# Optimization experiments

Hardware: AMD Instinct MI355X
Metric: run time of the kernel (lower is better)

Reference implementation:

```python
import jax, jax.numpy as jnp
import numpy as np
import math

B, N, OBS, H, A = 4096, 64, 64, 64, 8


def setup_inputs() -> dict:
    key = jax.random.key(0)
    kit = iter(jax.random.split(key, 64))

    def W(o, i):
        return jax.random.normal(next(kit), (o, i), jnp.float32) / float(np.sqrt(i))

    def bvec(o):
        return jax.random.normal(next(kit), (o,), jnp.float32) * 0.01

    inp = {
        "x": jax.random.normal(next(kit), (B, N, OBS), jnp.float32),
        "rnd_nums": jax.random.uniform(next(kit), (B, N), dtype=jnp.float32),
        "idx": jax.random.randint(next(kit), (B, N), 0, N),
    }
    inp.update(embed_w=W(H, OBS), embed_b=bvec(H))
    for pre in ("ia", "c1", "c2"):  # init_attn, consensus_attn1, consensus_attn2 (1 head)
        inp.update({pre + "_wq": W(H, H), pre + "_bq": bvec(H),
                    pre + "_wk": W(H, H), pre + "_bk": bvec(H),
                    pre + "_wv": W(H, H), pre + "_bv": bvec(H),
                    pre + "_wo": W(H, H), pre + "_bo": bvec(H)})
    inp.update(msg_w=W(H, H), msg_b=bvec(H), st_w=W(H, H), st_b=bvec(H),
               mean_w=W(A, 2 * H), mean_b=bvec(A), ls_w=W(A, 2 * H), ls_b=bvec(A))
    return inp


def reference(x, rnd_nums, idx, embed_w, embed_b,
              ia_wq, ia_bq, ia_wk, ia_bk, ia_wv, ia_bv, ia_wo, ia_bo,
              msg_w, msg_b, st_w, st_b,
              c1_wq, c1_bq, c1_wk, c1_bk, c1_wv, c1_bv, c1_wo, c1_bo,
              c2_wq, c2_bq, c2_wk, c2_bk, c2_wv, c2_bv, c2_wo, c2_bo,
              mean_w, mean_b, ls_w, ls_b):
    h = embed_w.shape[0]
    scale = 1.0 / math.sqrt(h)
    lrelu = lambda z: jax.nn.leaky_relu(z, 0.2)

    # ---- initial state estimation (self-attention over agents) ----
    e = lrelu(x @ embed_w.T + embed_b)                       # [B,N,H]
    q = e @ ia_wq.T + ia_bq
    k = e @ ia_wk.T + ia_bk
    v = e @ ia_wv.T + ia_bv
    w = jax.nn.softmax(jnp.einsum('bih,bjh->bij', q, k) * scale, axis=-1)
    attn = jnp.tanh(jnp.einsum('bij,bjh->bih', w, v) @ ia_wo.T + ia_bo)
    messages = attn @ msg_w.T + msg_b                        # [B,N,H]
    temp = attn @ st_w.T + st_b                              # [B,N,H]

    # ---- consensus masks: mg[b,i,j] = (r_i > a_i) | (r_j > a_i) ----
    a = jnp.take_along_axis(rnd_nums, idx, axis=1)           # agent_rnd per agent slot [B,N]
    gi = rnd_nums[:, :, None] > a[:, :, None]
    gj = rnd_nums[:, None, :] > a[:, :, None]
    mg = (gi | gj).astype(x.dtype)                           # [B,N,N]
    ml = 1.0 - mg

    def cons(mask, wq, bq, wk, bk, wv, bv, wo, bo):
        # single-token query (agent temp state) attends over zero-masked messages;
        # masked tokens contribute k = bk, v = bv (bias survives the zeroing).
        qq = temp @ wq.T + bq                                # [B,N,H]
        km = messages @ wk.T                                 # [B,N,H] (no bias; folded below)
        vm = messages @ wv.T
        s = (mask * jnp.einsum('bih,bjh->bij', qq, km) + (qq @ bk)[:, :, None]) * scale
        wgt = jax.nn.softmax(s, axis=-1)                     # [B,N_agents,N_tokens]
        ctx = jnp.einsum('bij,bjh->bih', wgt * mask, vm) + bv
        return ctx @ wo.T + bo

    o1 = cons(mg, c1_wq, c1_bq, c1_wk, c1_bk, c1_wv, c1_bv, c1_wo, c1_bo)
    o2 = cons(ml, c2_wq, c2_bq, c2_wk, c2_bk, c2_wv, c2_bv, c2_wo, c2_bo)
    out = lrelu(jnp.concatenate([o1, o2], axis=-1))          # [B,N,2H]
    mean = out @ mean_w.T + mean_b                           # [B,N,A]
    logstd = jnp.clip(out @ ls_w.T + ls_b, -20.0, 2.0)
    return mean, jnp.exp(logstd)
```

## Files before the change

### kernel.cpp

```cpp
#include <hip/hip_runtime.h>

namespace {

typedef __bf16 bf16x8 __attribute__((ext_vector_type(8)));
typedef float f32x4 __attribute__((ext_vector_type(4)));
typedef unsigned int uint4v __attribute__((ext_vector_type(4)));

#define MFMA16(a,b,c) __builtin_amdgcn_mfma_f32_16x16x32_bf16((a),(b),(c),0,0,0)

constexpr float SCALE = 0.125f;

constexpr int WS_HW  = 57344;
constexpr int WS_NV  = 61440;
constexpr int WS_VEC = 63488;
constexpr int WS_SC  = 65536;

__device__ __forceinline__ int PI(int c){ return 4*(c&15) + (c>>4); }
__device__ __forceinline__ int PINV(int p){ return 16*(p&3) + (p>>2); }

__device__ __forceinline__ unsigned short f2b(float f){
  return __builtin_bit_cast(unsigned short, (__bf16)f);
}
__device__ __forceinline__ unsigned pack2(float a, float b){
  return (unsigned)f2b(a) | ((unsigned)f2b(b)<<16);
}
template<int ACT>
__device__ __forceinline__ float actf(float v){
  if constexpr (ACT==1) return v>0.f ? v : 0.2f*v;
  else if constexpr (ACT==2) return 1.f - 2.f/(__expf(2.f*v)+1.f);
  else return v;
}

__device__ __forceinline__ void bar_lgkm(){
  asm volatile("s_waitcnt lgkmcnt(0)\n\ts_barrier" ::: "memory");
}
__device__ __forceinline__ void bar_full(){
  asm volatile("s_waitcnt vmcnt(0) lgkmcnt(0)\n\ts_barrier" ::: "memory");
}

struct PrepP {
  const float *embed_w, *mean_w, *ls_w;
  const float *ia_wq, *ia_bq, *ia_wk, *ia_wv, *ia_wo, *ia_bv, *ia_bo;
  const float *c1_wq, *c1_bq, *c1_wk, *c1_bk, *c1_wv, *c1_bv, *c1_wo, *c1_bo;
  const float *c2_wq, *c2_bq, *c2_wk, *c2_bk, *c2_wv, *c2_bv, *c2_wo, *c2_bo;
  const float *msg_w, *msg_b, *st_w, *st_b;
  char* ws;
};

__device__ void mmAB_f32(const float* A, const float* B, float* O){
  const int t=threadIdx.x, r=t>>2, c0=(t&3)*16;
  float acc[16];
  #pragma unroll
  for(int j=0;j<16;j++) acc[j]=0.f;
  for(int h=0;h<64;h++){
    const float a=A[r*64+h];
    #pragma unroll
    for(int j=0;j<16;j++) acc[j]=fmaf(a,B[h*64+c0+j],acc[j]);
  }
  #pragma unroll
  for(int j=0;j<16;j++) O[r*64+c0+j]=acc[j];
}
__device__ void mmAB_bf(const float* A, const float* B, __bf16* D){
  const int t=threadIdx.x, r=t>>2, c0=(t&3)*16;
  float acc[16];
  #pragma unroll
  for(int j=0;j<16;j++) acc[j]=0.f;
  for(int h=0;h<64;h++){
    const float a=A[r*64+h];
    #pragma unroll
    for(int j=0;j<16;j++) acc[j]=fmaf(a,B[h*64+c0+j],acc[j]);
  }
  #pragma unroll
  for(int j=0;j<16;j++) D[r*64+PI(c0+j)]=(__bf16)acc[j];
}
__device__ void mmTA_bfx(const float* A, const float* B, __bf16* D){
  const int t=threadIdx.x, a=t>>2, b0=(t&3)*16;
  float acc[16];
  #pragma unroll
  for(int j=0;j<16;j++) acc[j]=0.f;
  for(int h=0;h<64;h++){
    const float av=A[h*64+a];
    #pragma unroll
    for(int j=0;j<16;j++) acc[j]=fmaf(av,B[h*64+b0+j],acc[j]);
  }
  #pragma unroll
  for(int j=0;j<16;j++) D[a*64 + (PI(b0+j) ^ ((a&7)<<3))]=(__bf16)acc[j];
}

__global__ void prep_kernel(PrepP q){
  __shared__ float PF[2][4096];
  __shared__ float hv[64], gv[64];
  const int job=blockIdx.x, t=threadIdx.x;
  char* ws=q.ws;
  float* VECF=(float*)(ws+WS_VEC);
  float* SCF =(float*)(ws+WS_SC);
  __bf16* NVD=(__bf16*)(ws+WS_NV);

  if(job==0){
    __bf16* emb=(__bf16*)(ws+0*8192);
    #pragma unroll
    for(int i=0;i<16;i++){
      const int idx=t*16+i, o=idx>>6, pp=idx&63;
      emb[idx]=(__bf16)q.embed_w[o*64 + PINV(pp ^ ((o&7)<<3))];
    }
    __bf16* hw=(__bf16*)(ws+WS_HW);
    #pragma unroll
    for(int i=0;i<8;i++){
      const int flat=t*8+i, o=flat>>7, qq=flat&127, half=qq>>6, pp=qq&63;
      const float v=(o<8)?q.mean_w[o*128+half*64+PINV(pp)]
                         :q.ls_w[(o-8)*128+half*64+PINV(pp)];
      hw[flat]=(__bf16)v;
    }
    #pragma unroll
    for(int i=0;i<3;i++){ const int id=t*3+i; if(id<768) NVD[256+id]=(__bf16)0.f; }
  } else if(job==1){
    mmTA_bfx(q.ia_wk, q.ia_wq, (__bf16*)(ws+1*8192));
    if(t<64){ float s=0; for(int h=0;h<64;h++) s+=q.ia_wk[h*64+t]*q.ia_bq[h]; VECF[t]=s; }
  } else if(job==2){
    mmAB_bf(q.ia_wo, q.ia_wv, (__bf16*)(ws+2*8192));
    if(t<64){ float s=q.ia_bo[t]; for(int h=0;h<64;h++) s+=q.ia_wo[t*64+h]*q.ia_bv[h];
              VECF[64+t]=s; }
  } else if(job==3 || job==5){
    const int cons=(job==3)?0:1;
    const float *wq=cons?q.c2_wq:q.c1_wq, *bq=cons?q.c2_bq:q.c1_bq;
    const float *wk=cons?q.c2_wk:q.c1_wk, *bk=cons?q.c2_bk:q.c1_bk;
    mmAB_f32(wq, q.st_w, PF[0]);
    if(t<64){ float s=bq[t]; for(int k=0;k<64;k++) s+=wq[t*64+k]*q.st_b[k]; hv[t]=s; }
    __syncthreads();
    mmAB_f32(wk, q.msg_w, PF[1]);
    if(t<64){ float s=0; for(int k=0;k<64;k++) s+=wk[t*64+k]*q.msg_b[k]; gv[t]=s; }
    __syncthreads();
    mmTA_bfx(PF[1], PF[0], (__bf16*)(ws+(cons?5:3)*8192));
    if(t<64){
      float s=0; for(int h=0;h<64;h++) s+=PF[1][h*64+t]*hv[h];
      VECF[128+cons*64+t]=s;
      float s0=0,s1=0;
      for(int h=0;h<64;h++){ s0+=PF[0][h*64+t]*gv[h]; s1+=PF[0][h*64+t]*bk[h]; }
      NVD[(2*cons  )*64+PI(t)]=(__bf16)s0;
      NVD[(2*cons+1)*64+PI(t)]=(__bf16)s1;
    }
    if(t==0){
      float c=0,hb=0;
      for(int i=0;i<64;i++){ c+=hv[i]*gv[i]; hb+=hv[i]*bk[i]; }
      SCF[2*cons]=c; SCF[2*cons+1]=hb;
    }
  } else {
    const int cons=(job==4)?0:1;
    const float *wo=cons?q.c2_wo:q.c1_wo, *wvv=cons?q.c2_wv:q.c1_wv;
    const float *bv=cons?q.c2_bv:q.c1_bv, *bo=cons?q.c2_bo:q.c1_bo;
    mmAB_f32(wo, wvv, PF[0]);
    if(t<64){ float s=bo[t]; for(int h=0;h<64;h++) s+=wo[t*64+h]*bv[h];
              VECF[320+cons*128+t]=s; }
    __syncthreads();
    mmAB_bf(PF[0], q.msg_w, (__bf16*)(ws+(cons?6:4)*8192));
    if(t<64){ float s=0; for(int k=0;k<64;k++) s+=PF[0][t*64+k]*q.msg_b[k];
              VECF[256+cons*128+t]=s; }
  }
}

struct Params {
  const float *x, *rnd; const int *idx;
  const float *embed_b, *mean_b, *ls_b;
  const char* ws; float* out; int std_off;
};

__device__ __forceinline__ bf16x8 fragld(const char* buf, int row, int kb){
  const int byte = row*128 + (kb ^ ((row&7)<<4));
  return __builtin_bit_cast(bf16x8, *reinterpret_cast<const uint4v*>(buf + byte));
}
__device__ __forceinline__ bf16x8 gld(const char* a){
  return __builtin_bit_cast(bf16x8, *reinterpret_cast<const uint4v*>(a));
}
__device__ __forceinline__ void stageT(const char* src, char* L, int t){
  __builtin_amdgcn_global_load_lds(
      (const __attribute__((address_space(1))) unsigned int*)(src + t*16),
      (__attribute__((address_space(3))) unsigned int*)(L + (t>>6)*1024), 16, 0, 0);
}
__device__ __forceinline__ void loadB_lds(const char* Bl, bf16x8* bf, int fr, int fg){
  #pragma unroll
  for(int n=0;n<4;n++){
    bf[2*n]   = fragld(Bl, n*16+fr, fg*16);
    bf[2*n+1] = fragld(Bl, n*16+fr, 64+fg*16);
  }
}

__device__ __forceinline__ void mm_AB(const char* A, const char* Bl, f32x4* acc,
                                      int fr,int fg,int wv4){
  const bf16x8 a0=fragld(A,16*wv4+fr,fg*16), a1=fragld(A,16*wv4+fr,64+fg*16);
  #pragma unroll
  for(int n=0;n<4;n++){
    acc[n]=MFMA16(a0, fragld(Bl,n*16+fr,fg*16),    acc[n]);
    acc[n]=MFMA16(a1, fragld(Bl,n*16+fr,64+fg*16), acc[n]);
  }
}
__device__ __forceinline__ void mm_rAB(bf16x8 a0, bf16x8 a1, const bf16x8* bf,
                                       f32x4* acc){
  #pragma unroll
  for(int n=0;n<4;n++){
    acc[n]=MFMA16(a0, bf[2*n],   acc[n]);
    acc[n]=MFMA16(a1, bf[2*n+1], acc[n]);
  }
}

template<int ACT>
__device__ __forceinline__ void store_cb(char* C, const f32x4* acc, const float* bz,
                                         int fr,int fg,int wv4){
  #pragma unroll
  for(int r=0;r<4;r++){
    const int R=16*wv4+4*fg+r;
    float v[4];
    #pragma unroll
    for(int n=0;n<4;n++) v[n]=actf<ACT>(acc[n][r]+bz[n]);
    uint2 pk; pk.x=pack2(v[0],v[1]); pk.y=pack2(v[2],v[3]);
    *reinterpret_cast<uint2*>(C + R*128 + ((8*fr)^((R&7)<<4))) = pk;
  }
}
__device__ __forceinline__ void store_rb(char* C, const f32x4* acc, const float* dR,
                                         int fr,int fg,int wv4){
  #pragma unroll
  for(int r=0;r<4;r++){
    const int R=16*wv4+4*fg+r;
    float v[4];
    #pragma unroll
    for(int n=0;n<4;n++) v[n]=acc[n][r]+dR[r];
    uint2 pk; pk.x=pack2(v[0],v[1]); pk.y=pack2(v[2],v[3]);
    *reinterpret_cast<uint2*>(C + R*128 + ((8*fr)^((R&7)<<4))) = pk;
  }
}

template<int MODE>
__device__ __forceinline__ void ssoft(const char* Aq, const bf16x8* bf, char* P,
                                      const float* rs, const float* as_,
                                      const float* zu, const float* zq,
                                      float cu, float cq,
                                      int fr,int fg,int wv4){
  f32x4 acc[4];
  #pragma unroll
  for(int n=0;n<4;n++) acc[n]=f32x4{0.f,0.f,0.f,0.f};
  const bf16x8 a0=fragld(Aq,16*wv4+fr,fg*16), a1=fragld(Aq,16*wv4+fr,64+fg*16);
  #pragma unroll
  for(int n=0;n<4;n++){
    acc[n]=MFMA16(a0, bf[2*n],   acc[n]);
    acc[n]=MFMA16(a1, bf[2*n+1], acc[n]);
  }
  unsigned mbits=0;
  if constexpr(MODE!=0){
    float rc[4], aR[4], ucR[4], qtR[4]; bool giR[4];
    #pragma unroll
    for(int n=0;n<4;n++) rc[n]=rs[n*16+fr];
    #pragma unroll
    for(int r=0;r<4;r++){
      const int R=16*wv4+4*fg+r;
      aR[r]=as_[R]; giR[r]=rs[R]>aR[r];
      ucR[r]=zu[R]+cu; qtR[r]=zq[R]+cq;
    }
    #pragma unroll
    for(int n=0;n<4;n++){
      #pragma unroll
      for(int r=0;r<4;r++){
        bool mv=giR[r]||(rc[n]>aR[r]);
        if constexpr(MODE==2) mv=!mv;
        const float mf=mv?1.f:0.f;
        if(mv) mbits|=1u<<(n*4+r);
        acc[n][r]=(mf*(acc[n][r]+ucR[r])+qtR[r])*SCALE;
      }
    }
  }
  float sm[4]={0,0,0,0};
  #pragma unroll
  for(int n=0;n<4;n++){
    #pragma unroll
    for(int r=0;r<4;r++){
      float e;
      if constexpr(MODE==0) e=__expf(acc[n][r]*SCALE);
      else e=__expf(acc[n][r]);
      acc[n][r]=e; sm[r]+=e;
    }
  }
  #pragma unroll
  for(int m=1;m<16;m<<=1){
    #pragma unroll
    for(int r=0;r<4;r++) sm[r]+=__shfl_xor(sm[r],m);
  }
  #pragma unroll
  for(int r=0;r<4;r++){
    const int R=16*wv4+4*fg+r;
    const float ri=1.f/sm[r];
    float v[4];
    #pragma unroll
    for(int n=0;n<4;n++){
      float e=acc[n][r]*ri;
      if constexpr(MODE!=0) e=(mbits&(1u<<(n*4+r)))?e:0.f;
      v[n]=e;
    }
    uint2 pk; pk.x=pack2(v[0],v[1]); pk.y=pack2(v[2],v[3]);
    *reinterpret_cast<uint2*>(P + R*128 + ((8*fr)^((R&7)<<4))) = pk;
  }
}

__global__ __launch_bounds__(512,4) void rap_kernel(Params p, int Bb){
  __shared__ __align__(16) char Bact[2][3][8192];
  __shared__ __align__(16) char WSst[2][8192];
  __shared__ float rnd_s[2][64], a_s[2][64], zbuf[2][4][64];
  const int t=threadIdx.x;
  const int fr=t&15, fg=(t>>4)&3, wv=t>>6, l=t&63;
  const int item=wv>>2, wv4=wv&3;
  const int b0=blockIdx.x*2;
  const int bi=(b0+item<Bb)?(b0+item):(Bb-1);
  const char* ws=p.ws;
  const float* VECF=(const float*)(ws+WS_VEC);
  const float* SCF =(const float*)(ws+WS_SC);
  char* A0=Bact[item][0]; char* A1=Bact[item][1]; char* A2=Bact[item][2];
  char* WO1=WSst[item];
  bf16x8 bfv[8];

  stageT(ws+0*8192, WSst[0], t);
  stageT(ws+1*8192, WSst[1], t);
  if(t<128){
    const int it2=t>>6, i2=t&63;
    const int bb=(b0+it2<Bb)?(b0+it2):(Bb-1);
    rnd_s[it2][i2]=p.rnd[bb*64+i2];
    a_s[it2][i2]  =p.rnd[bb*64+p.idx[bb*64+i2]];
  }
  {
    const float* Gx=p.x+(size_t)bi*4096;
    #pragma unroll
    for(int j=0;j<2;j++){
      const int lf=j*64+l, R=16*wv4+(lf>>3), k=lf&7;
      const float2 L0=*reinterpret_cast<const float2*>(Gx+R*64+2*k);
      const float2 L1=*reinterpret_cast<const float2*>(Gx+R*64+16+2*k);
      const float2 L2=*reinterpret_cast<const float2*>(Gx+R*64+32+2*k);
      const float2 L3=*reinterpret_cast<const float2*>(Gx+R*64+48+2*k);
      uint4 pk;
      pk.x=pack2(L0.x,L1.x); pk.y=pack2(L2.x,L3.x);
      pk.z=pack2(L0.y,L1.y); pk.w=pack2(L2.y,L3.y);
      *reinterpret_cast<uint4*>(A0 + R*128 + ((16*k)^((R&7)<<4)))=pk;
    }
  }
  bar_full();
  { f32x4 acc[4]={{0,0,0,0},{0,0,0,0},{0,0,0,0},{0,0,0,0}};
    mm_AB(A0, WSst[0], acc, fr,fg,wv4);
    float bz[4];
    #pragma unroll
    for(int n=0;n<4;n++) bz[n]=p.embed_b[n*16+fr];
    store_cb<1>(A1, acc, bz, fr,fg,wv4); }
  { f32x4 acc[4]={{0,0,0,0},{0,0,0,0},{0,0,0,0},{0,0,0,0}};
    mm_AB(A1, WSst[1], acc, fr,fg,wv4);
    float bz[4];
    #pragma unroll
    for(int n=0;n<4;n++) bz[n]=VECF[n*16+fr];
    store_cb<0>(A0, acc, bz, fr,fg,wv4); }
  bar_lgkm();
  stageT(ws+3*8192, WSst[0], t);
  stageT(ws+5*8192, WSst[1], t);
  const bf16x8 aVo0=gld(ws+2*8192+(16*wv4+fr)*128+fg*16);
  const bf16x8 aVo1=gld(ws+2*8192+(16*wv4+fr)*128+64+fg*16);
  loadB_lds(A1, bfv, fr, fg);
  ssoft<0>(A0, bfv, A0, nullptr,nullptr,nullptr,nullptr,0.f,0.f, fr,fg,wv4);
  { f32x4 acc[4]={{0,0,0,0},{0,0,0,0},{0,0,0,0},{0,0,0,0}};
    mm_rAB(aVo0, aVo1, bfv, acc);
    const float bz[4]={0,0,0,0};
    store_cb<0>(A2, acc, bz, fr,fg,wv4); }
  bar_full();
  const bf16x8 nv0=gld(ws+WS_NV+fr*128+fg*16);
  const bf16x8 nv1=gld(ws+WS_NV+fr*128+64+fg*16);
  { f32x4 acc[4]={{0,0,0,0},{0,0,0,0},{0,0,0,0},{0,0,0,0}};
    mm_AB(A0, A2, acc, fr,fg,wv4);
    float bz[4];
    #pragma unroll
    for(int n=0;n<4;n++) bz[n]=VECF[64+n*16+fr];
    store_cb<2>(A1, acc, bz, fr,fg,wv4); }
  { const bf16x8 a0=fragld(A1,16*wv4+fr,fg*16), a1=fragld(A1,16*wv4+fr,64+fg*16);
    f32x4 acc[4]={{0,0,0,0},{0,0,0,0},{0,0,0,0},{0,0,0,0}};
    #pragma unroll
    for(int n=0;n<4;n++){
      acc[n]=MFMA16(a0, fragld(WSst[0],n*16+fr,fg*16),    acc[n]);
      acc[n]=MFMA16(a1, fragld(WSst[0],n*16+fr,64+fg*16), acc[n]);
    }
    f32x4 za={0,0,0,0};
    za=MFMA16(a0, nv0, za);
    za=MFMA16(a1, nv1, za);
    if(fr<4){
      #pragma unroll
      for(int r=0;r<4;r++) zbuf[item][fr][16*wv4+4*fg+r]=za[r];
    }
    float bz[4];
    #pragma unroll
    for(int n=0;n<4;n++) bz[n]=VECF[128+n*16+fr];
    store_cb<0>(A0, acc, bz, fr,fg,wv4); }
  bar_lgkm();
  const bf16x8 aN10=gld(ws+4*8192+(16*wv4+fr)*128+fg*16);
  const bf16x8 aN11=gld(ws+4*8192+(16*wv4+fr)*128+64+fg*16);
  loadB_lds(A1, bfv, fr, fg);
  ssoft<1>(A0, bfv, A0, rnd_s[item], a_s[item], zbuf[item][0], zbuf[item][1],
           SCF[0], SCF[1], fr,fg,wv4);
  { f32x4 acc[4]={{0,0,0,0},{0,0,0,0},{0,0,0,0},{0,0,0,0}};
    mm_rAB(aN10, aN11, bfv, acc);
    float dR[4];
    #pragma unroll
    for(int r=0;r<4;r++) dR[r]=VECF[256+16*wv4+4*fg+r];
    store_rb(A2, acc, dR, fr,fg,wv4); }
  bar_lgkm();
  f32x4 o1acc[4]={{0,0,0,0},{0,0,0,0},{0,0,0,0},{0,0,0,0}};
  mm_AB(A0, A2, o1acc, fr,fg,wv4);
  { f32x4 acc[4]={{0,0,0,0},{0,0,0,0},{0,0,0,0},{0,0,0,0}};
    const bf16x8 a0=fragld(A1,16*wv4+fr,fg*16), a1=fragld(A1,16*wv4+fr,64+fg*16);
    #pragma unroll
    for(int n=0;n<4;n++){
      acc[n]=MFMA16(a0, fragld(WSst[1],n*16+fr,fg*16),    acc[n]);
      acc[n]=MFMA16(a1, fragld(WSst[1],n*16+fr,64+fg*16), acc[n]);
    }
    float bz[4];
    #pragma unroll
    for(int n=0;n<4;n++) bz[n]=VECF[192+n*16+fr];
    store_cb<0>(A0, acc, bz, fr,fg,wv4); }
  bar_lgkm();
  { float bz[4];
    #pragma unroll
    for(int n=0;n<4;n++) bz[n]=VECF[320+n*16+fr];
    store_cb<1>(WO1, o1acc, bz, fr,fg,wv4); }
  const bf16x8 aN20=gld(ws+6*8192+(16*wv4+fr)*128+fg*16);
  const bf16x8 aN21=gld(ws+6*8192+(16*wv4+fr)*128+64+fg*16);
  loadB_lds(A1, bfv, fr, fg);
  ssoft<2>(A0, bfv, A0, rnd_s[item], a_s[item], zbuf[item][2], zbuf[item][3],
           SCF[2], SCF[3], fr,fg,wv4);
  { f32x4 acc[4]={{0,0,0,0},{0,0,0,0},{0,0,0,0},{0,0,0,0}};
    mm_rAB(aN20, aN21, bfv, acc);
    float dR[4];
    #pragma unroll
    for(int r=0;r<4;r++) dR[r]=VECF[384+16*wv4+4*fg+r];
    store_rb(A2, acc, dR, fr,fg,wv4); }
  bar_lgkm();
  bf16x8 hw[4];
  #pragma unroll
  for(int kt=0;kt<4;kt++) hw[kt]=gld(ws+WS_HW + fr*256 + kt*64 + fg*16);
  { f32x4 acc[4]={{0,0,0,0},{0,0,0,0},{0,0,0,0},{0,0,0,0}};
    mm_AB(A0, A2, acc, fr,fg,wv4);
    float bz[4];
    #pragma unroll
    for(int n=0;n<4;n++) bz[n]=VECF[448+n*16+fr];
    store_cb<1>(A1, acc, bz, fr,fg,wv4); }
  { f32x4 acc={0,0,0,0};
    #pragma unroll
    for(int kt=0;kt<4;kt++){
      const bf16x8 af=fragld(kt<2?WO1:A1, 16*wv4+fr, (kt&1)*64+fg*16);
      acc=MFMA16(af, hw[kt], acc);
    }
    if(b0+item<Bb){
      const float bz=(fr<8)?p.mean_b[fr]:p.ls_b[fr-8];
      #pragma unroll
      for(int r=0;r<4;r++){
        const int R=16*wv4+4*fg+r;
        const int g=((b0+item)*64+R)*8;
        float v=acc[r]+bz;
        if(fr<8) p.out[g+fr]=v;
        else{ v=fminf(fmaxf(v,-20.f),2.f); p.out[p.std_off+g+(fr-8)]=__expf(v); }
      }
    }
  }
}

}

extern "C" void kernel_launch(void* const* d_in, const int* in_sizes, int n_in,
                              void* d_out, int out_size, void* d_ws, size_t ws_size,
                              hipStream_t stream){
  (void)n_in; (void)out_size; (void)ws_size;
  PrepP q;
  q.embed_w=(const float*)d_in[3];
  q.ia_wq=(const float*)d_in[5];  q.ia_bq=(const float*)d_in[6];
  q.ia_wk=(const float*)d_in[7];
  q.ia_wv=(const float*)d_in[9];  q.ia_bv=(const float*)d_in[10];
  q.ia_wo=(const float*)d_in[11]; q.ia_bo=(const float*)d_in[12];
  q.c1_wq=(const float*)d_in[13]; q.c1_bq=(const float*)d_in[14];
  q.c1_wk=(const float*)d_in[15]; q.c1_bk=(const float*)d_in[16];
  q.c1_wv=(const float*)d_in[17]; q.c1_bv=(const float*)d_in[18];
  q.c1_wo=(const float*)d_in[19]; q.c1_bo=(const float*)d_in[20];
  q.c2_wq=(const float*)d_in[21]; q.c2_bq=(const float*)d_in[22];
  q.c2_wk=(const float*)d_in[23]; q.c2_bk=(const float*)d_in[24];
  q.c2_wv=(const float*)d_in[25]; q.c2_bv=(const float*)d_in[26];
  q.c2_wo=(const float*)d_in[27]; q.c2_bo=(const float*)d_in[28];
  q.msg_w=(const float*)d_in[29]; q.msg_b=(const float*)d_in[30];
  q.st_w =(const float*)d_in[31]; q.st_b =(const float*)d_in[32];
  q.mean_w=(const float*)d_in[33]; q.ls_w=(const float*)d_in[35];
  q.ws=(char*)d_ws;
  prep_kernel<<<dim3(7), dim3(256), 0, stream>>>(q);

  Params p;
  p.x  =(const float*)d_in[0];
  p.rnd=(const float*)d_in[1];
  p.idx=(const int*)  d_in[2];
  p.embed_b=(const float*)d_in[4];
  p.mean_b =(const float*)d_in[34];
  p.ls_b   =(const float*)d_in[36];
  p.ws=(const char*)d_ws;
  p.out=(float*)d_out;
  const int Bb=in_sizes[0]/4096;
  p.std_off=Bb*64*8;
  const int nb=(Bb+1)/2;
  rap_kernel<<<dim3(nb), dim3(512), 0, stream>>>(p, Bb);
}
```

Measured before the change: 115.8 us.

## Drop shared weight staging buffers, load consensus weights from global into registers

Removes the 16KB WSst shared buffer by staging the embed weights into the unused third activation slot, and loads consensus Q·K weight fragments straight from global into registers instead of LDS. The final head projection is split so the o1 part accumulates early, which frees the separate o1 buffer. Launch bounds go from 4 to 6 blocks per CU to use the reduced LDS footprint. The prep kernel's mmTA_bfx is replaced with an explicit per-thread loop that writes a permuted layout. This trades more global/L2 loads and register pressure for higher occupancy.

```diff
diff --git a/kernel.cpp b/kernel.cpp
--- a/kernel.cpp
+++ b/kernel.cpp
@@ -130,7 +130,19 @@
     mmAB_f32(wk, q.msg_w, PF[1]);
     if(t<64){ float s=0; for(int k=0;k<64;k++) s+=wk[t*64+k]*q.msg_b[k]; gv[t]=s; }
     __syncthreads();
-    mmTA_bfx(PF[1], PF[0], (__bf16*)(ws+(cons?5:3)*8192));
+    { const int a=t>>2, b0=(t&3)*16;
+      float acc[16];
+      #pragma unroll
+      for(int j=0;j<16;j++) acc[j]=0.f;
+      for(int h=0;h<64;h++){
+        const float av=PF[1][h*64+a];
+        #pragma unroll
+        for(int j=0;j<16;j++) acc[j]=fmaf(av,PF[0][h*64+b0+j],acc[j]);
+      }
+      __bf16* D=(__bf16*)(ws+(cons?5:3)*8192);
+      #pragma unroll
+      for(int j=0;j<16;j++) D[a*64+PI(b0+j)]=(__bf16)acc[j];
+    }
     if(t<64){
       float s=0; for(int h=0;h<64;h++) s+=PF[1][h*64+t]*hv[h];
       VECF[128+cons*64+t]=s;
@@ -183,6 +195,13 @@
     bf[2*n+1] = fragld(Bl, n*16+fr, 64+fg*16);
   }
 }
+__device__ __forceinline__ void loadB_gl(const char* W, bf16x8* bf, int fr, int fg){
+  #pragma unroll
+  for(int n=0;n<4;n++){
+    bf[2*n]   = gld(W + (n*16+fr)*128 + fg*16);
+    bf[2*n+1] = gld(W + (n*16+fr)*128 + 64 + fg*16);
+  }
+}
 
 __device__ __forceinline__ void mm_AB(const char* A, const char* Bl, f32x4* acc,
                                       int fr,int fg,int wv4){
@@ -191,6 +210,15 @@
   for(int n=0;n<4;n++){
     acc[n]=MFMA16(a0, fragld(Bl,n*16+fr,fg*16),    acc[n]);
     acc[n]=MFMA16(a1, fragld(Bl,n*16+fr,64+fg*16), acc[n]);
+  }
+}
+__device__ __forceinline__ void mm_ABr(const char* A, const bf16x8* bf, f32x4* acc,
+                                       int fr,int fg,int wv4){
+  const bf16x8 a0=fragld(A,16*wv4+fr,fg*16), a1=fragld(A,16*wv4+fr,64+fg*16);
+  #pragma unroll
+  for(int n=0;n<4;n++){
+    acc[n]=MFMA16(a0, bf[2*n],   acc[n]);
+    acc[n]=MFMA16(a1, bf[2*n+1], acc[n]);
   }
 }
 __device__ __forceinline__ void mm_rAB(bf16x8 a0, bf16x8 a1, const bf16x8* bf,
@@ -298,9 +326,8 @@
   }
 }
 
-__global__ __launch_bounds__(512,4) void rap_kernel(Params p, int Bb){
+__global__ __launch_bounds__(512,6) void rap_kernel(Params p, int Bb){
   __shared__ __align__(16) char Bact[2][3][8192];
-  __shared__ __align__(16) char WSst[2][8192];
   __shared__ float rnd_s[2][64], a_s[2][64], zbuf[2][4][64];
   const int t=threadIdx.x;
   const int fr=t&15, fg=(t>>4)&3, wv=t>>6, l=t&63;
@@ -311,11 +338,10 @@
   const float* VECF=(const float*)(ws+WS_VEC);
   const float* SCF =(const float*)(ws+WS_SC);
   char* A0=Bact[item][0]; char* A1=Bact[item][1]; char* A2=Bact[item][2];
-  char* WO1=WSst[item];
   bf16x8 bfv[8];
 
-  stageT(ws+0*8192, WSst[0], t);
-  stageT(ws+1*8192, WSst[1], t);
+  stageT(ws+0*8192, Bact[0][2], t);
+  stageT(ws+1*8192, Bact[1][2], t);
   if(t<128){
     const int it2=t>>6, i2=t&63;
     const int bb=(b0+it2<Bb)?(b0+it2):(Bb-1);
@@ -339,20 +365,18 @@
   }
   bar_full();
   { f32x4 acc[4]={{0,0,0,0},{0,0,0,0},{0,0,0,0},{0,0,0,0}};
-    mm_AB(A0, WSst[0], acc, fr,fg,wv4);
+    mm_AB(A0, Bact[0][2], acc, fr,fg,wv4);
     float bz[4];
     #pragma unroll
     for(int n=0;n<4;n++) bz[n]=p.embed_b[n*16+fr];
     store_cb<1>(A1, acc, bz, fr,fg,wv4); }
   { f32x4 acc[4]={{0,0,0,0},{0,0,0,0},{0,0,0,0},{0,0,0,0}};
-    mm_AB(A1, WSst[1], acc, fr,fg,wv4);
+    mm_AB(A1, Bact[1][2], acc, fr,fg,wv4);
     float bz[4];
     #pragma unroll
     for(int n=0;n<4;n++) bz[n]=VECF[n*16+fr];
     store_cb<0>(A0, acc, bz, fr,fg,wv4); }
   bar_lgkm();
-  stageT(ws+3*8192, WSst[0], t);
-  stageT(ws+5*8192, WSst[1], t);
   const bf16x8 aVo0=gld(ws+2*8192+(16*wv4+fr)*128+fg*16);
   const bf16x8 aVo1=gld(ws+2*8192+(16*wv4+fr)*128+64+fg*16);
   loadB_lds(A1, bfv, fr, fg);
@@ -361,9 +385,10 @@
     mm_rAB(aVo0, aVo1, bfv, acc);
     const float bz[4]={0,0,0,0};
     store_cb<0>(A2, acc, bz, fr,fg,wv4); }
-  bar_full();
+  bar_lgkm();
   const bf16x8 nv0=gld(ws+WS_NV+fr*128+fg*16);
   const bf16x8 nv1=gld(ws+WS_NV+fr*128+64+fg*16);
+  loadB_gl(ws+3*8192, bfv, fr, fg);
   { f32x4 acc[4]={{0,0,0,0},{0,0,0,0},{0,0,0,0},{0,0,0,0}};
     mm_AB(A0, A2, acc, fr,fg,wv4);
     float bz[4];
@@ -374,8 +399,8 @@
     f32x4 acc[4]={{0,0,0,0},{0,0,0,0},{0,0,0,0},{0,0,0,0}};
     #pragma unroll
     for(int n=0;n<4;n++){
-      acc[n]=MFMA16(a0, fragld(WSst[0],n*16+fr,fg*16),    acc[n]);
-      acc[n]=MFMA16(a1, fragld(WSst[0],n*16+fr,64+fg*16), acc[n]);
+      acc[n]=MFMA16(a0, bfv[2*n],   acc[n]);
+      acc[n]=MFMA16(a1, bfv[2*n+1], acc[n]);
     }
     f32x4 za={0,0,0,0};
     za=MFMA16(a0, nv0, za);
@@ -401,24 +426,25 @@
     for(int r=0;r<4;r++) dR[r]=VECF[256+16*wv4+4*fg+r];
     store_rb(A2, acc, dR, fr,fg,wv4); }
   bar_lgkm();
-  f32x4 o1acc[4]={{0,0,0,0},{0,0,0,0},{0,0,0,0},{0,0,0,0}};
-  mm_AB(A0, A2, o1acc, fr,fg,wv4);
-  { f32x4 acc[4]={{0,0,0,0},{0,0,0,0},{0,0,0,0},{0,0,0,0}};
-    const bf16x8 a0=fragld(A1,16*wv4+fr,fg*16), a1=fragld(A1,16*wv4+fr,64+fg*16);
-    #pragma unroll
-    for(int n=0;n<4;n++){
-      acc[n]=MFMA16(a0, fragld(WSst[1],n*16+fr,fg*16),    acc[n]);
-      acc[n]=MFMA16(a1, fragld(WSst[1],n*16+fr,64+fg*16), acc[n]);
-    }
+  loadB_gl(ws+5*8192, bfv, fr, fg);
+  const bf16x8 h0=gld(ws+WS_HW + fr*256 + 0*64 + fg*16);
+  const bf16x8 h1=gld(ws+WS_HW + fr*256 + 1*64 + fg*16);
+  f32x4 hacc={0,0,0,0};
+  { f32x4 o1acc[4]={{0,0,0,0},{0,0,0,0},{0,0,0,0},{0,0,0,0}};
+    mm_AB(A0, A2, o1acc, fr,fg,wv4);
+    float bz[4];
+    #pragma unroll
+    for(int n=0;n<4;n++) bz[n]=VECF[320+n*16+fr];
+    store_cb<1>(A0, o1acc, bz, fr,fg,wv4); }
+  hacc=MFMA16(fragld(A0,16*wv4+fr,fg*16),    h0, hacc);
+  hacc=MFMA16(fragld(A0,16*wv4+fr,64+fg*16), h1, hacc);
+  { f32x4 acc[4]={{0,0,0,0},{0,0,0,0},{0,0,0,0},{0,0,0,0}};
+    mm_ABr(A1, bfv, acc, fr,fg,wv4);
     float bz[4];
     #pragma unroll
     for(int n=0;n<4;n++) bz[n]=VECF[192+n*16+fr];
     store_cb<0>(A0, acc, bz, fr,fg,wv4); }
   bar_lgkm();
-  { float bz[4];
-    #pragma unroll
-    for(int n=0;n<4;n++) bz[n]=VECF[320+n*16+fr];
-    store_cb<1>(WO1, o1acc, bz, fr,fg,wv4); }
   const bf16x8 aN20=gld(ws+6*8192+(16*wv4+fr)*128+fg*16);
   const bf16x8 aN21=gld(ws+6*8192+(16*wv4+fr)*128+64+fg*16);
   loadB_lds(A1, bfv, fr, fg);
@@ -431,31 +457,25 @@
     for(int r=0;r<4;r++) dR[r]=VECF[384+16*wv4+4*fg+r];
     store_rb(A2, acc, dR, fr,fg,wv4); }
   bar_lgkm();
-  bf16x8 hw[4];
-  #pragma unroll
-  for(int kt=0;kt<4;kt++) hw[kt]=gld(ws+WS_HW + fr*256 + kt*64 + fg*16);
+  const bf16x8 h2=gld(ws+WS_HW + fr*256 + 2*64 + fg*16);
+  const bf16x8 h3=gld(ws+WS_HW + fr*256 + 3*64 + fg*16);
   { f32x4 acc[4]={{0,0,0,0},{0,0,0,0},{0,0,0,0},{0,0,0,0}};
     mm_AB(A0, A2, acc, fr,fg,wv4);
     float bz[4];
     #pragma unroll
     for(int n=0;n<4;n++) bz[n]=VECF[448+n*16+fr];
     store_cb<1>(A1, acc, bz, fr,fg,wv4); }
-  { f32x4 acc={0,0,0,0};
-    #pragma unroll
-    for(int kt=0;kt<4;kt++){
-      const bf16x8 af=fragld(kt<2?WO1:A1, 16*wv4+fr, (kt&1)*64+fg*16);
-      acc=MFMA16(af, hw[kt], acc);
-    }
-    if(b0+item<Bb){
-      const float bz=(fr<8)?p.mean_b[fr]:p.ls_b[fr-8];
-      #pragma unroll
-      for(int r=0;r<4;r++){
-        const int R=16*wv4+4*fg+r;
-        const int g=((b0+item)*64+R)*8;
-        float v=acc[r]+bz;
-        if(fr<8) p.out[g+fr]=v;
-        else{ v=fminf(fmaxf(v,-20.f),2.f); p.out[p.std_off+g+(fr-8)]=__expf(v); }
-      }
+  hacc=MFMA16(fragld(A1,16*wv4+fr,fg*16),    h2, hacc);
+  hacc=MFMA16(fragld(A1,16*wv4+fr,64+fg*16), h3, hacc);
+  if(b0+item<Bb){
+    const float bz=(fr<8)?p.mean_b[fr]:p.ls_b[fr-8];
+    #pragma unroll
+    for(int r=0;r<4;r++){
+      const int R=16*wv4+4*fg+r;
+      const int g=((b0+item)*64+R)*8;
+      float v=hacc[r]+bz;
+      if(fr<8) p.out[g+fr]=v;
+      else{ v=fminf(fmaxf(v,-20.f),2.f); p.out[p.std_off+g+(fr-8)]=__expf(v); }
     }
   }
 }
```

After: 158.8 us. 1.37x slower.
